# Kernel tuning notes

Hardware: AMD Instinct MI355X
Metric: run time of the kernel (lower is better)

## Reference

```python
import jax, jax.numpy as jnp
import numpy as np

N_ATOMS = 200
SEG_LEN = 1
N_FRAMES = 256


def _get_segments(n_atoms: int, length: int) -> np.ndarray:
    # All pairs of non-overlapping length-`length` segments [i, i+L, j, j+L], j - i > L.
    n_starts = n_atoms - length  # 199 segment start points
    i, j = np.triu_indices(n_starts, k=length + 1)
    return np.stack([i, i + length, j, j + length], axis=1).astype(np.int64)


def setup_inputs() -> dict:
    key = jax.random.key(0)
    xyz = jax.random.normal(key, (N_FRAMES, N_ATOMS, 3), dtype=jnp.float32) * 3.0
    segments = jnp.asarray(_get_segments(N_ATOMS, SEG_LEN))  # (19503, 4)
    return {"xyz": xyz, "segments": segments}


def _nnorm(x):
    return x / jnp.linalg.norm(x, axis=-1, keepdims=True)


def reference(xyz, segments):
    F = xyz.shape[0]
    S = segments.shape[0]
    # Gather the 4 endpoint coordinates per segment pair: (F, S, 4, 3)
    smat = xyz[:, segments]
    # displacements[a*2+b] = smat[2+b] - smat[a] for a,b in {0,1}: (F, S, 4, 3)
    disp = _nnorm((smat[:, :, None, 2:, :] - smat[:, :, :2, None, :]).reshape(F, S, 4, 3))
    idx_a = jnp.array([0, 1, 3, 2])
    idx_b = jnp.array([1, 3, 2, 0])
    crosses = _nnorm(jnp.cross(disp[:, :, idx_a], disp[:, :, idx_b]))  # (F, S, 4, 3)
    dots = jnp.sum(crosses * crosses[:, :, idx_b], axis=-1)  # (F, S, 4)
    omega = jnp.arcsin(jnp.clip(dots, -1.0, 1.0)).sum(-1)  # (F, S)
    signs = jnp.sign(
        jnp.sum(
            jnp.cross(smat[:, :, 3] - smat[:, :, 2], smat[:, :, 1] - smat[:, :, 0])
            * disp[:, :, 0],
            axis=-1,
        )
    )
    wr = (1.0 / (2.0 * jnp.pi)) * (omega * signs)
    return jnp.squeeze(wr)
```

## Files before the change

### kernel.cpp

```cpp
#include <hip/hip_runtime.h>
#include <math.h>

#define ATOMS 200

static __device__ __forceinline__ float3 f3(float x, float y, float z) {
    return make_float3(x, y, z);
}
static __device__ __forceinline__ float3 sub3(float3 a, float3 b) {
    return f3(a.x - b.x, a.y - b.y, a.z - b.z);
}
static __device__ __forceinline__ float dot3(float3 a, float3 b) {
    return fmaf(a.x, b.x, fmaf(a.y, b.y, a.z * b.z));
}
static __device__ __forceinline__ float3 cross3(float3 a, float3 b) {
    return f3(fmaf(a.y, b.z, -a.z * b.y),
              fmaf(a.z, b.x, -a.x * b.z),
              fmaf(a.x, b.y, -a.y * b.x));
}

static __device__ __forceinline__ float asin_fast(float x) {
    float a = fminf(fabsf(x), 1.0f);
    float t = __builtin_amdgcn_sqrtf(1.0f - a);
    float p = fmaf(a, -0.0187293f, 0.0742610f);
    p = fmaf(a, p, -0.2121144f);
    p = fmaf(a, p, 1.5707288f);
    return copysignf(fmaf(-t, p, 1.5707963267948966f), x);
}

__global__ __launch_bounds__(256) void writhe_kernel(
    const float* __restrict__ xyz,
    float*       __restrict__ out,
    int S, int m )
{
    __shared__ float sx[ATOMS * 3];

    const int f = blockIdx.y;
    const float* __restrict__ fx = xyz + (size_t)f * (ATOMS * 3);
    for (int t = threadIdx.x; t < (ATOMS * 3) / 2; t += 256)
        reinterpret_cast<float2*>(sx)[t] =
            reinterpret_cast<const float2*>(fx)[t];
    __syncthreads();

    const int s = blockIdx.x * blockDim.x + threadIdx.x;
    if (s >= S) return;

    const float mf = (float)m;
    const float sf = (float)s;
    const float tm = 2.0f * mf + 1.0f;
    const float disc = fmaf(tm, tm, -8.0f * sf);
    int i = (int)(0.5f * (tm - __builtin_amdgcn_sqrtf(disc)));
    i = max(0, min(i, m - 1));
    #define RBF(ii) fmaf((float)(ii), mf, -0.5f * (float)(ii) * ((float)(ii) - 1.0f))
    i += (int)(i < m - 1 && RBF(i + 1) <= sf);
    i += (int)(i < m - 1 && RBF(i + 1) <= sf);
    i -= (int)(i > 0 && RBF(i) > sf);
    const int j = i + 2 + (int)(sf - RBF(i));
    #undef RBF

    const float* ai = sx + 3 * i;
    const float* bj = sx + 3 * j;
    const float3 p0 = f3(ai[0], ai[1], ai[2]);
    const float3 p1 = f3(ai[3], ai[4], ai[5]);
    const float3 p2 = f3(bj[0], bj[1], bj[2]);
    const float3 p3 = f3(bj[3], bj[4], bj[5]);

    const float3 d0 = sub3(p2, p0), d1 = sub3(p3, p0);
    const float3 d2 = sub3(p2, p1), d3 = sub3(p3, p1);

    const float3 u0 = cross3(d0, d1);
    const float3 u1 = cross3(d1, d3);
    const float3 u3 = cross3(d2, d0);

    const float n0 = dot3(u0, u0);
    const float n1 = dot3(u1, u1);
    const float n3 = dot3(u3, u3);

    const float d01 = dot3(u0, u1) * __builtin_amdgcn_rsqf(n0 * n1);
    const float d13 = dot3(u1, u3) * __builtin_amdgcn_rsqf(n1 * n3);
    const float d30 = dot3(u3, u0) * __builtin_amdgcn_rsqf(n3 * n0);

    const float omega = asin_fast(d01) + asin_fast(d13) + asin_fast(d30)
                      + 1.5707963267948966f;

    const float sv = -dot3(u0, d2);
    float r = omega * 0.15915494309189535f;
    const unsigned rb = __float_as_uint(r) ^ (__float_as_uint(sv) & 0x80000000u);
    r = (sv == 0.0f) ? 0.0f : __uint_as_float(rb);

    out[(size_t)f * S + s] = r;
}

extern "C" void kernel_launch(void* const* d_in, const int* in_sizes, int n_in,
                              void* d_out, int out_size, void* d_ws, size_t ws_size,
                              hipStream_t stream)
{
    const float* xyz = (const float*)d_in[0];
    float*       out = (float*)d_out;

    const int F = in_sizes[0] / (ATOMS * 3);
    const int S = out_size / F;
    const int m = (int)((-1.0 + sqrt(1.0 + 8.0 * (double)S)) * 0.5 + 0.5);

    dim3 grid((S + 255) / 256, F);
    writhe_kernel<<<grid, 256, 0, stream>>>(xyz, out, S, m);
}
```

Before: 23.88 us.

## Process two frames per thread, read coordinates directly from global memory

Removes the shared-memory staging and block barrier, so each thread loads its two segment endpoint sextets straight from global memory (served from cache). Each thread now handles two frames, which spreads the index inversion (sqrt and corrections) over two outputs, and blocks grow to 1024 threads. The cost is unaligned 24-byte global gathers in place of LDS reads, and the code assumes F is divisible by FB, silently skipping the last frame when it is odd.

```diff
diff --git a/kernel.cpp b/kernel.cpp
--- a/kernel.cpp
+++ b/kernel.cpp
@@ -2,6 +2,8 @@
 #include <math.h>
 
 #define ATOMS 200
+#define FB 2
+#define BLK 1024
 
 static __device__ __forceinline__ float3 f3(float x, float y, float z) {
     return make_float3(x, y, z);
@@ -18,6 +20,8 @@
               fmaf(a.x, b.y, -a.y * b.x));
 }
 
+struct __attribute__((packed, aligned(4))) f6 { float v[6]; };
+
 static __device__ __forceinline__ float asin_fast(float x) {
     float a = fminf(fabsf(x), 1.0f);
     float t = __builtin_amdgcn_sqrtf(1.0f - a);
@@ -27,42 +31,11 @@
     return copysignf(fmaf(-t, p, 1.5707963267948966f), x);
 }
 
-__global__ __launch_bounds__(256) void writhe_kernel(
-    const float* __restrict__ xyz,
-    float*       __restrict__ out,
-    int S, int m )
-{
-    __shared__ float sx[ATOMS * 3];
-
-    const int f = blockIdx.y;
-    const float* __restrict__ fx = xyz + (size_t)f * (ATOMS * 3);
-    for (int t = threadIdx.x; t < (ATOMS * 3) / 2; t += 256)
-        reinterpret_cast<float2*>(sx)[t] =
-            reinterpret_cast<const float2*>(fx)[t];
-    __syncthreads();
-
-    const int s = blockIdx.x * blockDim.x + threadIdx.x;
-    if (s >= S) return;
-
-    const float mf = (float)m;
-    const float sf = (float)s;
-    const float tm = 2.0f * mf + 1.0f;
-    const float disc = fmaf(tm, tm, -8.0f * sf);
-    int i = (int)(0.5f * (tm - __builtin_amdgcn_sqrtf(disc)));
-    i = max(0, min(i, m - 1));
-    #define RBF(ii) fmaf((float)(ii), mf, -0.5f * (float)(ii) * ((float)(ii) - 1.0f))
-    i += (int)(i < m - 1 && RBF(i + 1) <= sf);
-    i += (int)(i < m - 1 && RBF(i + 1) <= sf);
-    i -= (int)(i > 0 && RBF(i) > sf);
-    const int j = i + 2 + (int)(sf - RBF(i));
-    #undef RBF
-
-    const float* ai = sx + 3 * i;
-    const float* bj = sx + 3 * j;
-    const float3 p0 = f3(ai[0], ai[1], ai[2]);
-    const float3 p1 = f3(ai[3], ai[4], ai[5]);
-    const float3 p2 = f3(bj[0], bj[1], bj[2]);
-    const float3 p3 = f3(bj[3], bj[4], bj[5]);
+static __device__ __forceinline__ float writhe_elem(const f6& A, const f6& B) {
+    const float3 p0 = f3(A.v[0], A.v[1], A.v[2]);
+    const float3 p1 = f3(A.v[3], A.v[4], A.v[5]);
+    const float3 p2 = f3(B.v[0], B.v[1], B.v[2]);
+    const float3 p3 = f3(B.v[3], B.v[4], B.v[5]);
 
     const float3 d0 = sub3(p2, p0), d1 = sub3(p3, p0);
     const float3 d2 = sub3(p2, p1), d3 = sub3(p3, p1);
@@ -85,9 +58,44 @@
     const float sv = -dot3(u0, d2);
     float r = omega * 0.15915494309189535f;
     const unsigned rb = __float_as_uint(r) ^ (__float_as_uint(sv) & 0x80000000u);
-    r = (sv == 0.0f) ? 0.0f : __uint_as_float(rb);
+    return (sv == 0.0f) ? 0.0f : __uint_as_float(rb);
+}
 
-    out[(size_t)f * S + s] = r;
+__global__ __launch_bounds__(BLK) void writhe_kernel(
+    const float* __restrict__ xyz,
+    float*       __restrict__ out,
+    int S, int m )
+{
+    const int s = blockIdx.x * BLK + threadIdx.x;
+    if (s >= S) return;
+    const int f0 = blockIdx.y * FB;
+
+    const float mf = (float)m;
+    const float sf = (float)s;
+    const float tm = 2.0f * mf + 1.0f;
+    const float disc = fmaf(tm, tm, -8.0f * sf);
+    int i = (int)(0.5f * (tm - __builtin_amdgcn_sqrtf(disc)));
+    i = max(0, min(i, m - 1));
+    #define RBF(ii) fmaf((float)(ii), mf, -0.5f * (float)(ii) * ((float)(ii) - 1.0f))
+    i += (int)(i < m - 1 && RBF(i + 1) <= sf);
+    i += (int)(i < m - 1 && RBF(i + 1) <= sf);
+    i -= (int)(i > 0 && RBF(i) > sf);
+    const int j = i + 2 + (int)(sf - RBF(i));
+    #undef RBF
+
+    const float* fx0 = xyz + (size_t)f0 * (ATOMS * 3);
+
+    const f6 A0 = *reinterpret_cast<const f6*>(fx0 + 3 * i);
+    const f6 B0 = *reinterpret_cast<const f6*>(fx0 + 3 * j);
+    const f6 A1 = *reinterpret_cast<const f6*>(fx0 + ATOMS * 3 + 3 * i);
+    const f6 B1 = *reinterpret_cast<const f6*>(fx0 + ATOMS * 3 + 3 * j);
+
+    const float r0 = writhe_elem(A0, B0);
+    const float r1 = writhe_elem(A1, B1);
+
+    float* o = out + (size_t)f0 * S + s;
+    o[0] = r0;
+    o[S] = r1;
 }
 
 extern "C" void kernel_launch(void* const* d_in, const int* in_sizes, int n_in,
@@ -101,6 +109,6 @@
     const int S = out_size / F;
     const int m = (int)((-1.0 + sqrt(1.0 + 8.0 * (double)S)) * 0.5 + 0.5);
 
-    dim3 grid((S + 255) / 256, F);
-    writhe_kernel<<<grid, 256, 0, stream>>>(xyz, out, S, m);
+    dim3 grid((S + BLK - 1) / BLK, F / FB);
+    writhe_kernel<<<grid, BLK, 0, stream>>>(xyz, out, S, m);
 }
```

Result: no change. 24.29 us (+1.7%).
